# Kernel optimization log

Measured on AMD Instinct MI355X. Metric: run time of the kernel, lower is better.

## Reference

```python
import jax, jax.numpy as jnp
import numpy as np

K = 24            # patch_size (window)
D = 4             # dilation
C = 256           # dim
H = 8             # num_heads
N = 500000        # number of octree tokens at this depth (nnum_t)
BATCH_SIZE = 8
BLOCK = K * D
NA = int(np.ceil(N / BLOCK)) * BLOCK   # nnum_a (padded length)
PAD = NA - N
SCALE = (C // H) ** -0.5
MASK_VAL = -1000.0


def setup_inputs() -> dict:
    key = jax.random.key(0)
    k1, k2, k3, k4 = jax.random.split(key, 4)
    data = jax.random.normal(k1, (N, C), jnp.float32)
    qkv_w = jax.random.normal(k2, (3 * C, C), jnp.float32) * 0.02
    qkv_b = jnp.zeros((3 * C,), jnp.float32)
    proj_w = jax.random.normal(k3, (C, C), jnp.float32) * 0.02
    proj_b = jnp.zeros((C,), jnp.float32)
    batch_idx = jnp.sort(jax.random.randint(k4, (N,), 0, BATCH_SIZE, dtype=jnp.int32))
    return {"data": data, "qkv_w": qkv_w, "qkv_b": qkv_b,
            "proj_w": proj_w, "proj_b": proj_b, "batch_idx": batch_idx}


def _dilate_mask(batch_idx):
    # patch_partition of batch ids: pad with fill_value = batch_size
    b = jnp.concatenate([batch_idx, jnp.full((PAD,), BATCH_SIZE, jnp.int32)], axis=0)
    # dilate reshuffle: (-1, K, D) -> transpose -> (-1, K) windows
    b = b.reshape(-1, K, D).transpose(0, 2, 1).reshape(-1, K)
    diff = b[:, :, None] - b[:, None, :]           # [nw, K, K]
    return jnp.where(diff != 0, MASK_VAL, 0.0).astype(jnp.float32)


def reference(data, qkv_w, qkv_b, proj_w, proj_b, batch_idx):
    mask = _dilate_mask(batch_idx)                              # [nw, K, K]
    # patch_partition of features: pad with zeros
    x = jnp.concatenate([data, jnp.zeros((PAD, C), data.dtype)], axis=0)
    # dilation reshuffle: (-1, K, D, C) -> (-1, D, K, C) -> windows [nw, K, C]
    x = x.reshape(-1, K, D, C).transpose(0, 2, 1, 3).reshape(-1, K, C)
    qkv = (x @ qkv_w.T + qkv_b).reshape(-1, K, 3, H, C // H).transpose(2, 0, 3, 1, 4)
    q, k, v = qkv[0] * SCALE, qkv[1], qkv[2]                    # [nw, H, K, hd]
    attn = jnp.einsum('nhqd,nhkd->nhqk', q, k) + mask[:, None]  # [nw, H, K, K]
    attn = jax.nn.softmax(attn, axis=-1)
    out = jnp.einsum('nhqk,nhkd->nhqd', attn, v)
    out = out.transpose(0, 2, 1, 3).reshape(-1, C)              # merge heads
    # reverse dilation reshuffle, drop padding (patch_reverse)
    out = out.reshape(-1, D, K, C).transpose(0, 2, 1, 3).reshape(-1, C)[:N]
    return out @ proj_w.T + proj_b
```

## Files before the change

### kernel.cpp

```cpp
#include <hip/hip_runtime.h>


#define N_TOK 500000
#define NA    500064
#define MP    500096
#define CDIM  256
#define KWIN  24
#define NWIN  20836
#define HEADS 8
#define SCALE_F 0.17677669529663689f

typedef __attribute__((ext_vector_type(8))) short bf16x8;
typedef __attribute__((ext_vector_type(4))) float f32x4;

__device__ __forceinline__ unsigned short f2b(float f) {
    unsigned int u = __float_as_uint(f);
    u += 0x7fffu + ((u >> 16) & 1u);
    return (unsigned short)(u >> 16);
}

#define GLOAD_LDS16(gsrc, ldst) \
    __builtin_amdgcn_global_load_lds((const __attribute__((address_space(1))) void*)(gsrc), \
                                     (__attribute__((address_space(3))) void*)(ldst), 16, 0, 0)


__global__ __launch_bounds__(256) void cvt_data_kernel(const float* __restrict__ src,
                                                       unsigned short* __restrict__ dst) {
    long long i = (long long)blockIdx.x * 256 + threadIdx.x;
    long long base = i * 8;
    int row = (int)(base >> 8);
    uint4 o;
    if (row < N_TOK) {
        float4 a = *(const float4*)(src + base);
        float4 b = *(const float4*)(src + base + 4);
        o.x = (unsigned)f2b(a.x) | ((unsigned)f2b(a.y) << 16);
        o.y = (unsigned)f2b(a.z) | ((unsigned)f2b(a.w) << 16);
        o.z = (unsigned)f2b(b.x) | ((unsigned)f2b(b.y) << 16);
        o.w = (unsigned)f2b(b.z) | ((unsigned)f2b(b.w) << 16);
    } else {
        o = make_uint4(0u, 0u, 0u, 0u);
    }
    *(uint4*)(dst + base) = o;
}

__global__ __launch_bounds__(256) void cvt_w_kernel(const float* __restrict__ src,
                                                    unsigned short* __restrict__ dst, int n8) {
    int i = blockIdx.x * 256 + threadIdx.x;
    if (i >= n8) return;
    float4 a = ((const float4*)src)[i * 2];
    float4 b = ((const float4*)src)[i * 2 + 1];
    uint4 o;
    o.x = (unsigned)f2b(a.x) | ((unsigned)f2b(a.y) << 16);
    o.y = (unsigned)f2b(a.z) | ((unsigned)f2b(a.w) << 16);
    o.z = (unsigned)f2b(b.x) | ((unsigned)f2b(b.y) << 16);
    o.w = (unsigned)f2b(b.z) | ((unsigned)f2b(b.w) << 16);
    ((uint4*)dst)[i] = o;
}

__global__ __launch_bounds__(256) void zero_pad_kernel(unsigned short* __restrict__ dst) {
    int i = blockIdx.x * 256 + threadIdx.x;
    if (i < (MP - N_TOK) * CDIM / 8)
        *(uint4*)(dst + (size_t)N_TOK * CDIM + (size_t)i * 8) = make_uint4(0u, 0u, 0u, 0u);
}


template<int NN, bool OUT_F32>
__global__ __launch_bounds__(256, 2) void gemm_kernel(const unsigned short* __restrict__ A,
                                                      const unsigned short* __restrict__ Bt,
                                                      const float* __restrict__ bias,
                                                      void* __restrict__ out_p,
                                                      int m_write) {
    __shared__ unsigned short ldsA[128 * 64];
    __shared__ unsigned short ldsB[128 * 64];
    const int tid  = threadIdx.x;
    const int lane = tid & 63;
    const int wv   = tid >> 6;
    const int wr   = wv >> 1, wc = wv & 1;
    const int mtile = blockIdx.y, ntile = blockIdx.x;

    f32x4 acc[4][4];
    #pragma unroll
    for (int i = 0; i < 4; ++i) {
        #pragma unroll
        for (int j = 0; j < 4; ++j) {
            #pragma unroll
            for (int r = 0; r < 4; ++r) acc[i][j][r] = 0.f;
        }
    }

    const char* abase = (const char*)(A  + (size_t)mtile * 128 * CDIM);
    const char* bbase = (const char*)(Bt + (size_t)ntile * 128 * CDIM);
    const int lrow8 = lane >> 3;
    const int lcolb = (lane & 7) * 16;

    for (int kt = 0; kt < 4; ++kt) {
        const int kb_byte = kt * 128;
        #pragma unroll
        for (int c = 0; c < 4; ++c) {
            int chunk = wv * 4 + c;
            int row = chunk * 8 + lrow8;
            GLOAD_LDS16(abase + (size_t)row * 512 + kb_byte + lcolb, &ldsA[chunk * 512]);
        }
        #pragma unroll
        for (int c = 0; c < 4; ++c) {
            int chunk = wv * 4 + c;
            int row = chunk * 8 + lrow8;
            GLOAD_LDS16(bbase + (size_t)row * 512 + kb_byte + lcolb, &ldsB[chunk * 512]);
        }
        __syncthreads();
        #pragma unroll
        for (int ks = 0; ks < 2; ++ks) {
            const int kb = ks * 32 + (lane >> 4) * 8;
            bf16x8 af[4], bfr[4];
            #pragma unroll
            for (int i = 0; i < 4; ++i) {
                af[i]  = *(const bf16x8*)&ldsA[(wr * 64 + i * 16 + (lane & 15)) * 64 + kb];
                bfr[i] = *(const bf16x8*)&ldsB[(wc * 64 + i * 16 + (lane & 15)) * 64 + kb];
            }
            #pragma unroll
            for (int i = 0; i < 4; ++i) {
                #pragma unroll
                for (int j = 0; j < 4; ++j)
                    acc[i][j] = __builtin_amdgcn_mfma_f32_16x16x32_bf16(af[i], bfr[j], acc[i][j], 0, 0, 0);
            }
        }
        __syncthreads();
    }

    #pragma unroll
    for (int i = 0; i < 4; ++i) {
        int row0 = mtile * 128 + wr * 64 + i * 16 + ((lane >> 4) << 2);
        #pragma unroll
        for (int j = 0; j < 4; ++j) {
            int col = ntile * 128 + wc * 64 + j * 16 + (lane & 15);
            float bv = bias[col];
            #pragma unroll
            for (int r = 0; r < 4; ++r) {
                int row = row0 + r;
                float v = acc[i][j][r] + bv;
                if (OUT_F32) {
                    if (row < m_write) ((float*)out_p)[(size_t)row * NN + col] = v;
                } else {
                    ((unsigned short*)out_p)[(size_t)row * NN + col] = f2b(v);
                }
            }
        }
    }
}


__global__ __launch_bounds__(256) void attn_kernel(const unsigned short* __restrict__ qkv,
                                                   const int* __restrict__ batch_idx,
                                                   unsigned short* __restrict__ attn_out) {
    __shared__ unsigned short sP[4][32 * 64];
    const int tid  = threadIdx.x;
    const int lane = tid & 63;
    const int ws_  = tid >> 6;
    const int wid  = blockIdx.x * 4 + ws_;
    const int w = wid >> 3, h = wid & 7;
    const int gw = w >> 2, dd = w & 3;
    const int lrow = lane & 15, lg = lane >> 4;
    const int pbase = gw * 96 + dd;

    bf16x8 Qf[2], Kf[2];
    #pragma unroll
    for (int t = 0; t < 2; ++t) {
        size_t p = (size_t)(pbase + (t * 16 + lrow) * 4);
        const unsigned short* bp = qkv + p * 768 + h * 32 + lg * 8;
        Qf[t] = *(const bf16x8*)bp;
        Kf[t] = *(const bf16x8*)(bp + 256);
    }

    unsigned short v0[8], v1[8];
    #pragma unroll
    for (int j2 = 0; j2 < 8; ++j2) {
        size_t p = (size_t)(pbase + (lg * 8 + j2) * 4);
        const unsigned short* vp = qkv + p * 768 + 512 + h * 32 + lrow;
        v0[j2] = vp[0];
        v1[j2] = vp[16];
    }

    int bq[2];
    #pragma unroll
    for (int j = 0; j < 2; ++j) {
        int r = j * 16 + lrow;
        int p = pbase + r * 4;
        bq[j] = (r < KWIN && p < N_TOK) ? batch_idx[p] : -1;
    }
    int bk[2][4];
    #pragma unroll
    for (int i = 0; i < 2; ++i)
        #pragma unroll
        for (int rr = 0; rr < 4; ++rr) {
            int r = i * 16 + lg * 4 + rr;
            int p = pbase + r * 4;
            bk[i][rr] = (r < KWIN && p < N_TOK) ? batch_idx[p] : -2;
        }

    f32x4 accS[2][2];
    #pragma unroll
    for (int i = 0; i < 2; ++i)
        #pragma unroll
        for (int j = 0; j < 2; ++j)
            #pragma unroll
            for (int r = 0; r < 4; ++r) accS[i][j][r] = 0.f;
    #pragma unroll
    for (int i = 0; i < 2; ++i)
        #pragma unroll
        for (int j = 0; j < 2; ++j)
            accS[i][j] = __builtin_amdgcn_mfma_f32_16x16x32_bf16(Kf[i], Qf[j], accS[i][j], 0, 0, 0);

    float sv[2][2][4];
    float mx[2] = { -3.0e38f, -3.0e38f };
    #pragma unroll
    for (int i = 0; i < 2; ++i)
        #pragma unroll
        for (int j = 0; j < 2; ++j)
            #pragma unroll
            for (int rr = 0; rr < 4; ++rr) {
                float val = (bk[i][rr] == bq[j]) ? accS[i][j][rr] * SCALE_F : -1.0e9f;
                sv[i][j][rr] = val;
                mx[j] = fmaxf(mx[j], val);
            }
    mx[0] = fmaxf(mx[0], __shfl_xor(mx[0], 16)); mx[0] = fmaxf(mx[0], __shfl_xor(mx[0], 32));
    mx[1] = fmaxf(mx[1], __shfl_xor(mx[1], 16)); mx[1] = fmaxf(mx[1], __shfl_xor(mx[1], 32));
    float sm[2] = { 0.f, 0.f };
    #pragma unroll
    for (int i = 0; i < 2; ++i)
        #pragma unroll
        for (int j = 0; j < 2; ++j)
            #pragma unroll
            for (int rr = 0; rr < 4; ++rr) {
                float e = __expf(sv[i][j][rr] - mx[j]);
                sv[i][j][rr] = e;
                sm[j] += e;
            }
    sm[0] += __shfl_xor(sm[0], 16); sm[0] += __shfl_xor(sm[0], 32);
    sm[1] += __shfl_xor(sm[1], 16); sm[1] += __shfl_xor(sm[1], 32);
    float inv[2] = { 1.f / sm[0], 1.f / sm[1] };

    char* pb = (char*)sP[ws_];
    const int swz = (lrow & 7) << 4;
    #pragma unroll
    for (int j = 0; j < 2; ++j) {
        int q = j * 16 + lrow;
        #pragma unroll
        for (int i = 0; i < 2; ++i) {
            unsigned lo = (unsigned)f2b(sv[i][j][0] * inv[j]) | ((unsigned)f2b(sv[i][j][1] * inv[j]) << 16);
            unsigned hi = (unsigned)f2b(sv[i][j][2] * inv[j]) | ((unsigned)f2b(sv[i][j][3] * inv[j]) << 16);
            *(uint2*)(pb + q * 128 + ((i * 32 + lg * 8) ^ swz)) = make_uint2(lo, hi);
        }
    }
    bf16x8 AP[2];
    #pragma unroll
    for (int jj = 0; jj < 2; ++jj)
        AP[jj] = *(const bf16x8*)(pb + (jj * 16 + lrow) * 128 + ((lg * 16) ^ swz));

    union { bf16x8 v; unsigned short s[8]; } B0, B1;
    #pragma unroll
    for (int j2 = 0; j2 < 8; ++j2) { B0.s[j2] = v0[j2]; B1.s[j2] = v1[j2]; }
    f32x4 accO[2][2];
    #pragma unroll
    for (int i = 0; i < 2; ++i)
        #pragma unroll
        for (int j = 0; j < 2; ++j)
            #pragma unroll
            for (int r = 0; r < 4; ++r) accO[i][j][r] = 0.f;
    #pragma unroll
    for (int jj = 0; jj < 2; ++jj) {
        accO[jj][0] = __builtin_amdgcn_mfma_f32_16x16x32_bf16(AP[jj], B0.v, accO[jj][0], 0, 0, 0);
        accO[jj][1] = __builtin_amdgcn_mfma_f32_16x16x32_bf16(AP[jj], B1.v, accO[jj][1], 0, 0, 0);
    }

    #pragma unroll
    for (int jj = 0; jj < 2; ++jj)
        #pragma unroll
        for (int rr = 0; rr < 4; ++rr) {
            int q = jj * 16 + lg * 4 + rr;
            int p = pbase + q * 4;
            if (q < KWIN && p < N_TOK) {
                unsigned short* op = attn_out + (size_t)p * CDIM + h * 32;
                op[lrow]      = f2b(accO[jj][0][rr]);
                op[16 + lrow] = f2b(accO[jj][1][rr]);
            }
        }
}


extern "C" void kernel_launch(void* const* d_in, const int* in_sizes, int n_in,
                              void* d_out, int out_size, void* d_ws, size_t ws_size,
                              hipStream_t stream) {
    const float* data    = (const float*)d_in[0];
    const float* qkv_w   = (const float*)d_in[1];
    const float* qkv_b   = (const float*)d_in[2];
    const float* proj_w  = (const float*)d_in[3];
    const float* proj_b  = (const float*)d_in[4];
    const int*   batch_i = (const int*)d_in[5];

    char* ws = (char*)d_ws;
    size_t off = 0;
    unsigned short* dataB  = (unsigned short*)(ws + off); off += (size_t)MP * CDIM * 2;
    unsigned short* qkvB   = (unsigned short*)(ws + off); off += (size_t)MP * 768 * 2;
    unsigned short* attnB  = (unsigned short*)(ws + off); off += (size_t)MP * CDIM * 2;
    unsigned short* wqkvB  = (unsigned short*)(ws + off); off += (size_t)768 * 256 * 2;
    unsigned short* wprojB = (unsigned short*)(ws + off); off += (size_t)256 * 256 * 2;
    if (ws_size < off) return;

    cvt_data_kernel<<<MP / 8, 256, 0, stream>>>(data, dataB);
    cvt_w_kernel<<<(768 * 256 / 8 + 255) / 256, 256, 0, stream>>>(qkv_w, wqkvB, 768 * 256 / 8);
    cvt_w_kernel<<<(256 * 256 / 8 + 255) / 256, 256, 0, stream>>>(proj_w, wprojB, 256 * 256 / 8);
    zero_pad_kernel<<<12, 256, 0, stream>>>(attnB);

    gemm_kernel<768, false><<<dim3(6, MP / 128), 256, 0, stream>>>(dataB, wqkvB, qkv_b, qkvB, MP);
    attn_kernel<<<NWIN * HEADS / 4, 256, 0, stream>>>(qkvB, batch_i, attnB);
    gemm_kernel<256, true><<<dim3(2, MP / 128), 256, 0, stream>>>(attnB, wprojB, proj_b, d_out, N_TOK);
}
```

Before: 1.007 ms.

## Fuse fp32-to-bf16 input conversion into QKV GEMM and remap block tiles

Drops the separate pass that converted the whole input to bf16. The QKV GEMM now reads fp32 rows directly, converts them in registers and stores them to LDS, which saves a full write and re-read of the bf16 copy. The GEMM grids are linearised so that groups of 8 M-tiles share each N-tile, which should improve L2 reuse, and the occupancy hint rises to 3 blocks per CU. In exchange the A operand is loaded through registers rather than by direct-to-LDS loads, and each fp32 row is read and converted six times, once per N-tile.

```diff
diff --git a/kernel.cpp b/kernel.cpp
--- a/kernel.cpp
+++ b/kernel.cpp
@@ -4,6 +4,8 @@
 #define N_TOK 500000
 #define NA    500064
 #define MP    500096
+#define MT    3907
+#define MT8   3912
 #define CDIM  256
 #define KWIN  24
 #define NWIN  20836
@@ -23,25 +25,6 @@
     __builtin_amdgcn_global_load_lds((const __attribute__((address_space(1))) void*)(gsrc), \
                                      (__attribute__((address_space(3))) void*)(ldst), 16, 0, 0)
 
-
-__global__ __launch_bounds__(256) void cvt_data_kernel(const float* __restrict__ src,
-                                                       unsigned short* __restrict__ dst) {
-    long long i = (long long)blockIdx.x * 256 + threadIdx.x;
-    long long base = i * 8;
-    int row = (int)(base >> 8);
-    uint4 o;
-    if (row < N_TOK) {
-        float4 a = *(const float4*)(src + base);
-        float4 b = *(const float4*)(src + base + 4);
-        o.x = (unsigned)f2b(a.x) | ((unsigned)f2b(a.y) << 16);
-        o.y = (unsigned)f2b(a.z) | ((unsigned)f2b(a.w) << 16);
-        o.z = (unsigned)f2b(b.x) | ((unsigned)f2b(b.y) << 16);
-        o.w = (unsigned)f2b(b.z) | ((unsigned)f2b(b.w) << 16);
-    } else {
-        o = make_uint4(0u, 0u, 0u, 0u);
-    }
-    *(uint4*)(dst + base) = o;
-}
 
 __global__ __launch_bounds__(256) void cvt_w_kernel(const float* __restrict__ src,
                                                     unsigned short* __restrict__ dst, int n8) {
@@ -64,29 +47,115 @@
 }
 
 
-template<int NN, bool OUT_F32>
-__global__ __launch_bounds__(256, 2) void gemm_kernel(const unsigned short* __restrict__ A,
-                                                      const unsigned short* __restrict__ Bt,
-                                                      const float* __restrict__ bias,
-                                                      void* __restrict__ out_p,
-                                                      int m_write) {
+__global__ __launch_bounds__(256, 3) void qkv_gemm_kernel(const float* __restrict__ A32,
+                                                          const unsigned short* __restrict__ Bt,
+                                                          const float* __restrict__ bias,
+                                                          unsigned short* __restrict__ out) {
     __shared__ unsigned short ldsA[128 * 64];
     __shared__ unsigned short ldsB[128 * 64];
+    const int l = blockIdx.x;
+    const int s = l >> 3;
+    const int mtile = (l & 7) + 8 * (s / 6);
+    const int ntile = s - (s / 6) * 6;
+    if (mtile >= MT) return;
+
     const int tid  = threadIdx.x;
     const int lane = tid & 63;
     const int wv   = tid >> 6;
     const int wr   = wv >> 1, wc = wv & 1;
-    const int mtile = blockIdx.y, ntile = blockIdx.x;
 
     f32x4 acc[4][4];
     #pragma unroll
+    for (int i = 0; i < 4; ++i)
+        #pragma unroll
+        for (int j = 0; j < 4; ++j)
+            #pragma unroll
+            for (int r = 0; r < 4; ++r) acc[i][j][r] = 0.f;
+
+    const float* abase = A32 + (size_t)mtile * 128 * CDIM;
+    const char*  bbase = (const char*)(Bt + (size_t)ntile * 128 * CDIM);
+    const int lrow8 = lane >> 3;
+    const int lcolb = (lane & 7) * 16;
+    const int arow  = tid >> 4;
+    const int acol  = (tid & 15) * 4;
+    const int growb = mtile * 128;
+
+    for (int kt = 0; kt < 4; ++kt) {
+        #pragma unroll
+        for (int c = 0; c < 4; ++c) {
+            int chunk = wv * 4 + c;
+            int row = chunk * 8 + lrow8;
+            GLOAD_LDS16(bbase + (size_t)row * 512 + kt * 128 + lcolb, &ldsB[chunk * 512]);
+        }
+        #pragma unroll
+        for (int i = 0; i < 8; ++i) {
+            int row = i * 16 + arow;
+            float4 a = make_float4(0.f, 0.f, 0.f, 0.f);
+            if (growb + row < N_TOK)
+                a = *(const float4*)(abase + (size_t)row * CDIM + kt * 64 + acol);
+            uint2 o;
+            o.x = (unsigned)f2b(a.x) | ((unsigned)f2b(a.y) << 16);
+            o.y = (unsigned)f2b(a.z) | ((unsigned)f2b(a.w) << 16);
+            *(uint2*)&ldsA[row * 64 + acol] = o;
+        }
+        __syncthreads();
+        #pragma unroll
+        for (int ks = 0; ks < 2; ++ks) {
+            const int kb = ks * 32 + (lane >> 4) * 8;
+            bf16x8 af[4], bfr[4];
+            #pragma unroll
+            for (int i = 0; i < 4; ++i) {
+                af[i]  = *(const bf16x8*)&ldsA[(wr * 64 + i * 16 + (lane & 15)) * 64 + kb];
+                bfr[i] = *(const bf16x8*)&ldsB[(wc * 64 + i * 16 + (lane & 15)) * 64 + kb];
+            }
+            #pragma unroll
+            for (int i = 0; i < 4; ++i)
+                #pragma unroll
+                for (int j = 0; j < 4; ++j)
+                    acc[i][j] = __builtin_amdgcn_mfma_f32_16x16x32_bf16(af[i], bfr[j], acc[i][j], 0, 0, 0);
+        }
+        __syncthreads();
+    }
+
+    #pragma unroll
     for (int i = 0; i < 4; ++i) {
+        int row0 = mtile * 128 + wr * 64 + i * 16 + ((lane >> 4) << 2);
         #pragma unroll
         for (int j = 0; j < 4; ++j) {
+            int col = ntile * 128 + wc * 64 + j * 16 + (lane & 15);
+            float bv = bias[col];
+            #pragma unroll
+            for (int r = 0; r < 4; ++r)
+                out[(size_t)(row0 + r) * 768 + col] = f2b(acc[i][j][r] + bv);
+        }
+    }
+}
+
+
+__global__ __launch_bounds__(256, 3) void proj_gemm_kernel(const unsigned short* __restrict__ A,
+                                                           const unsigned short* __restrict__ Bt,
+                                                           const float* __restrict__ bias,
+                                                           float* __restrict__ out) {
+    __shared__ unsigned short ldsA[128 * 64];
+    __shared__ unsigned short ldsB[128 * 64];
+    const int l = blockIdx.x;
+    const int s = l >> 3;
+    const int mtile = (l & 7) + 8 * (s >> 1);
+    const int ntile = s & 1;
+    if (mtile >= MT) return;
+
+    const int tid  = threadIdx.x;
+    const int lane = tid & 63;
+    const int wv   = tid >> 6;
+    const int wr   = wv >> 1, wc = wv & 1;
+
+    f32x4 acc[4][4];
+    #pragma unroll
+    for (int i = 0; i < 4; ++i)
+        #pragma unroll
+        for (int j = 0; j < 4; ++j)
             #pragma unroll
             for (int r = 0; r < 4; ++r) acc[i][j][r] = 0.f;
-        }
-    }
 
     const char* abase = (const char*)(A  + (size_t)mtile * 128 * CDIM);
     const char* bbase = (const char*)(Bt + (size_t)ntile * 128 * CDIM);
@@ -118,11 +187,10 @@
                 bfr[i] = *(const bf16x8*)&ldsB[(wc * 64 + i * 16 + (lane & 15)) * 64 + kb];
             }
             #pragma unroll
-            for (int i = 0; i < 4; ++i) {
+            for (int i = 0; i < 4; ++i)
                 #pragma unroll
                 for (int j = 0; j < 4; ++j)
                     acc[i][j] = __builtin_amdgcn_mfma_f32_16x16x32_bf16(af[i], bfr[j], acc[i][j], 0, 0, 0);
-            }
         }
         __syncthreads();
     }
@@ -137,12 +205,7 @@
             #pragma unroll
             for (int r = 0; r < 4; ++r) {
                 int row = row0 + r;
-                float v = acc[i][j][r] + bv;
-                if (OUT_F32) {
-                    if (row < m_write) ((float*)out_p)[(size_t)row * NN + col] = v;
-                } else {
-                    ((unsigned short*)out_p)[(size_t)row * NN + col] = f2b(v);
-                }
+                if (row < N_TOK) out[(size_t)row * CDIM + col] = acc[i][j][r] + bv;
             }
         }
     }
@@ -299,19 +362,17 @@
 
     char* ws = (char*)d_ws;
     size_t off = 0;
-    unsigned short* dataB  = (unsigned short*)(ws + off); off += (size_t)MP * CDIM * 2;
     unsigned short* qkvB   = (unsigned short*)(ws + off); off += (size_t)MP * 768 * 2;
     unsigned short* attnB  = (unsigned short*)(ws + off); off += (size_t)MP * CDIM * 2;
     unsigned short* wqkvB  = (unsigned short*)(ws + off); off += (size_t)768 * 256 * 2;
     unsigned short* wprojB = (unsigned short*)(ws + off); off += (size_t)256 * 256 * 2;
     if (ws_size < off) return;
 
-    cvt_data_kernel<<<MP / 8, 256, 0, stream>>>(data, dataB);
     cvt_w_kernel<<<(768 * 256 / 8 + 255) / 256, 256, 0, stream>>>(qkv_w, wqkvB, 768 * 256 / 8);
     cvt_w_kernel<<<(256 * 256 / 8 + 255) / 256, 256, 0, stream>>>(proj_w, wprojB, 256 * 256 / 8);
     zero_pad_kernel<<<12, 256, 0, stream>>>(attnB);
 
-    gemm_kernel<768, false><<<dim3(6, MP / 128), 256, 0, stream>>>(dataB, wqkvB, qkv_b, qkvB, MP);
+    qkv_gemm_kernel<<<MT8 * 6, 256, 0, stream>>>(data, wqkvB, qkv_b, qkvB);
     attn_kernel<<<NWIN * HEADS / 4, 256, 0, stream>>>(qkvB, batch_i, attnB);
-    gemm_kernel<256, true><<<dim3(2, MP / 128), 256, 0, stream>>>(attnB, wprojB, proj_b, d_out, N_TOK);
-}
+    proj_gemm_kernel<<<MT8 * 2, 256, 0, stream>>>(attnB, wprojB, proj_b, (float*)d_out);
+}
```

New measurement: 1.344 ms. 1.33x slower.
